# Performance work log

Measured on AMD Instinct MI355X. Metric: run time of the kernel, lower is better.

The kernel has to match this reference:

```python
import jax, jax.numpy as jnp
import numpy as np

BN_EPS = 1e-5
DIST_MIN = 1e-10


def _three_nn(p1t, p2t):
    # p1t: [B,N,3], p2t: [B,S,3] -> squared dists/idx of 3 nearest, [B,N,3]
    d2 = (jnp.sum(p1t * p1t, -1, keepdims=True)
          - 2.0 * jnp.einsum('bnc,bsc->bns', p1t, p2t)
          + jnp.sum(p2t * p2t, -1)[:, None, :])  # [B,N,S]
    neg, idx = jax.lax.top_k(-d2, 3)
    return -neg, idx


def _gather_knn(f2t, idx):
    # f2t: [B,S,D], idx: [B,N,3] -> [B,N,3,D]
    return jax.vmap(lambda f, i: f[i])(f2t, idx)


def _conv_bn_relu(x, W, b, g, beta):
    # x: [B,C,N]; 1x1 conv == channel GEMM, then train-mode BN, then ReLU
    y = jnp.einsum('oc,bcn->bon', W, x) + b[None, :, None]
    mean = jnp.mean(y, axis=(0, 2), keepdims=True)
    var = jnp.mean((y - mean) ** 2, axis=(0, 2), keepdims=True)
    yn = (y - mean) * jax.lax.rsqrt(var + BN_EPS)
    return jax.nn.relu(yn * g[None, :, None] + beta[None, :, None])


def setup_inputs() -> dict:
    key = jax.random.key(0)
    ks = jax.random.split(key, 10)
    B, N, S, D1, D2 = 4, 8192, 2048, 128, 256
    C_in, C_mid, C_out = D1 + D2, 256, 256
    inp = {
        'pos1': jax.random.normal(ks[0], (B, 3, N), jnp.float32),
        'pos2': jax.random.normal(ks[1], (B, 3, S), jnp.float32),
        'feature1': jax.random.normal(ks[2], (B, D1, N), jnp.float32),
        'feature2': jax.random.normal(ks[3], (B, D2, S), jnp.float32),
        'W1': jax.random.normal(ks[4], (C_mid, C_in), jnp.float32) / np.sqrt(C_in),
        'b1': jnp.zeros((C_mid,), jnp.float32),
        'g1': jnp.ones((C_mid,), jnp.float32),
        'beta1': jnp.zeros((C_mid,), jnp.float32),
        'W2': jax.random.normal(ks[5], (C_out, C_mid), jnp.float32) / np.sqrt(C_mid),
        'b2': jnp.zeros((C_out,), jnp.float32),
        'g2': jnp.ones((C_out,), jnp.float32),
        'beta2': jnp.zeros((C_out,), jnp.float32),
    }
    return inp


def reference(pos1, pos2, feature1, feature2, W1, b1, g1, beta1, W2, b2, g2, beta2):
    B = pos1.shape[0]
    p1t = jnp.transpose(pos1, (0, 2, 1))  # [B,N,3]
    p2t = jnp.transpose(pos2, (0, 2, 1))  # [B,S,3]
    dists, idx = _three_nn(p1t, p2t)      # [B,N,3]
    dists = jnp.maximum(dists, DIST_MIN)
    w = 1.0 / dists
    w = w / jnp.sum(w, -1, keepdims=True)  # [B,N,3]
    f2t = jnp.transpose(feature2, (0, 2, 1))  # [B,S,D2]
    gathered = _gather_knn(f2t, idx)           # [B,N,3,D2]
    interp = jnp.sum(gathered * w[..., None], axis=2)  # [B,N,D2]
    interp = jnp.transpose(interp, (0, 2, 1))          # [B,D2,N]
    feat = jnp.concatenate([interp, feature1], axis=1)  # [B,D2+D1,N]
    feat = _conv_bn_relu(feat, W1, b1, g1, beta1)
    feat = _conv_bn_relu(feat, W2, b2, g2, beta2)
    return feat
```

## Files before the change

kernel.cpp:

```cpp
#include <hip/hip_runtime.h>
#include <hip/hip_bf16.h>

constexpr int B = 4, N = 8192, S = 2048;

typedef __attribute__((ext_vector_type(8))) short short8;
typedef __attribute__((ext_vector_type(4))) float v4f;

__device__ inline float u2f(ushort u) {
    union { ushort u; __hip_bfloat16 h; } c; c.u = u; return __bfloat162float(c.h);
}
__device__ inline ushort f2u(float f) {
    union { ushort u; __hip_bfloat16 h; } c; c.h = __float2bfloat16(f); return c.u;
}
__device__ inline void async_lds16(const void* g, void* l) {
    __builtin_amdgcn_global_load_lds(
        (const __attribute__((address_space(1))) unsigned*)g,
        (__attribute__((address_space(3))) unsigned*)l, 16, 0, 0);
}
__device__ inline short8 ld8(const ushort* p) { return *(const short8*)p; }

__global__ __launch_bounds__(256) void prep_kernel(
    const float* __restrict__ W1, const float* __restrict__ W2,
    __hip_bfloat16* __restrict__ W1r, __hip_bfloat16* __restrict__ W2r,
    float* __restrict__ zero_region)
{
    int i = blockIdx.x * 256 + threadIdx.x;
    if (i < 12288) {
        int kk = i >> 10, q = (i >> 8) & 3, o = i & 255;
        const float* src = W1 + o * 384 + kk * 32 + q * 8;
        float4 a = *(const float4*)src, b = *(const float4*)(src + 4);
        union { short8 s; ushort u[8]; } pk;
        pk.u[0] = f2u(a.x); pk.u[1] = f2u(a.y); pk.u[2] = f2u(a.z); pk.u[3] = f2u(a.w);
        pk.u[4] = f2u(b.x); pk.u[5] = f2u(b.y); pk.u[6] = f2u(b.z); pk.u[7] = f2u(b.w);
        *(short8*)((ushort*)W1r + i * 8) = pk.s;
    } else if (i < 20480) {
        int u = i - 12288;
        int kk = u >> 10, q = (u >> 8) & 3, o = u & 255;
        const float* src = W2 + o * 256 + kk * 32 + q * 8;
        float4 a = *(const float4*)src, b = *(const float4*)(src + 4);
        union { short8 s; ushort u[8]; } pk;
        pk.u[0] = f2u(a.x); pk.u[1] = f2u(a.y); pk.u[2] = f2u(a.z); pk.u[3] = f2u(a.w);
        pk.u[4] = f2u(b.x); pk.u[5] = f2u(b.y); pk.u[6] = f2u(b.z); pk.u[7] = f2u(b.w);
        *(short8*)((ushort*)W2r + u * 8) = pk.s;
    } else if (i < 21504) {
        zero_region[i - 20480] = 0.f;
    }
}

__global__ __launch_bounds__(256) void knn_kernel(
    const float* __restrict__ pos1, const float* __restrict__ pos2,
    float* __restrict__ wgt, int* __restrict__ idxb)
{
    __shared__ float4 p2s[S];
    const int b = blockIdx.y;
    for (int s = threadIdx.x; s < S; s += 256) {
        float x = pos2[(b * 3 + 0) * S + s];
        float y = pos2[(b * 3 + 1) * S + s];
        float z = pos2[(b * 3 + 2) * S + s];
        p2s[s] = make_float4(x, y, z, x * x + y * y + z * z);
    }
    __syncthreads();

    const int qi = blockIdx.x * 16 + (threadIdx.x >> 4);
    const int lp = threadIdx.x & 15;
    const float x1 = pos1[(b * 3 + 0) * N + qi];
    const float y1 = pos1[(b * 3 + 1) * N + qi];
    const float z1 = pos1[(b * 3 + 2) * N + qi];
    const float t1 = x1 * x1 + y1 * y1 + z1 * z1;

    float d0 = 3.4e38f, d1 = 3.4e38f, d2 = 3.4e38f;
    int i0 = 0x7fffffff, i1 = 0x7fffffff, i2 = 0x7fffffff;

    for (int tt = 0; tt < S / 16; ++tt) {
        int s = 16 * tt + lp;
        float4 p = p2s[s];
        float dot = x1 * p.x + y1 * p.y + z1 * p.z;
        float dd = (t1 - 2.0f * dot) + p.w;
        bool c0 = dd < d0, c1 = dd < d1, c2 = dd < d2;
        d2 = c1 ? d1 : (c2 ? dd : d2);
        i2 = c1 ? i1 : (c2 ? s : i2);
        d1 = c0 ? d0 : (c1 ? dd : d1);
        i1 = c0 ? i0 : (c1 ? s : i1);
        d0 = c0 ? dd : d0;
        i0 = c0 ? s : i0;
    }

    #pragma unroll
    for (int m = 1; m <= 8; m <<= 1) {
        float c0 = __shfl_xor(d0, m), c1 = __shfl_xor(d1, m), c2 = __shfl_xor(d2, m);
        int   j0 = __shfl_xor(i0, m), j1 = __shfl_xor(i1, m), j2 = __shfl_xor(i2, m);
        float cd[3] = {c0, c1, c2};
        int   cj[3] = {j0, j1, j2};
        #pragma unroll
        for (int k = 0; k < 3; ++k) {
            float d = cd[k]; int id = cj[k];
            bool l0 = (d < d0) || (d == d0 && id < i0);
            bool l1 = (d < d1) || (d == d1 && id < i1);
            bool l2 = (d < d2) || (d == d2 && id < i2);
            if (l0)      { d2 = d1; i2 = i1; d1 = d0; i1 = i0; d0 = d; i0 = id; }
            else if (l1) { d2 = d1; i2 = i1; d1 = d; i1 = id; }
            else if (l2) { d2 = d; i2 = id; }
        }
    }

    if (lp == 0) {
        float w0 = 1.f / fmaxf(d0, 1e-10f);
        float w1 = 1.f / fmaxf(d1, 1e-10f);
        float w2 = 1.f / fmaxf(d2, 1e-10f);
        float inv = 1.f / (w0 + w1 + w2);
        i0 = ((unsigned)i0 < S) ? i0 : 0;
        i1 = ((unsigned)i1 < S) ? i1 : 0;
        i2 = ((unsigned)i2 < S) ? i2 : 0;
        int base = (b * N + qi) * 3;
        wgt[base + 0] = w0 * inv; wgt[base + 1] = w1 * inv; wgt[base + 2] = w2 * inv;
        idxb[base + 0] = i0; idxb[base + 1] = i1; idxb[base + 2] = i2;
    }
}

__global__ __launch_bounds__(256) void transpose_k(
    const float* __restrict__ in, __hip_bfloat16* __restrict__ out,
    int L, int C)
{
    __shared__ ushort tl[64][66];
    const int b = blockIdx.z;
    const int l0 = blockIdx.x * 64, c0 = blockIdx.y * 64;
    const int t = threadIdx.x;
    const float* ip = in + (size_t)b * C * L;
    const int lr = t & 63, cb = t >> 6;
    #pragma unroll
    for (int i = 0; i < 16; ++i) {
        int c = cb + 4 * i;
        tl[lr][c] = f2u(ip[(size_t)(c0 + c) * L + l0 + lr]);
    }
    __syncthreads();
    ushort* op = (ushort*)out + (size_t)b * L * C;
    const int cp = t & 31, lrow = t >> 5;
    #pragma unroll
    for (int i = 0; i < 8; ++i) {
        int l = lrow + 8 * i;
        ushort2 v;
        v.x = tl[l][2 * cp];
        v.y = tl[l][2 * cp + 1];
        *(ushort2*)(op + (size_t)(l0 + l) * C + c0 + 2 * cp) = v;
    }
}

__global__ __launch_bounds__(256) void gemm1_kernel(
    const __hip_bfloat16* __restrict__ Wr, const float* __restrict__ bias,
    const __hip_bfloat16* __restrict__ f2T, const __hip_bfloat16* __restrict__ f1T,
    const int* __restrict__ idxb, const float* __restrict__ wgt,
    __hip_bfloat16* __restrict__ y, float* __restrict__ sums)
{
    __shared__ __align__(16) ushort Xs[64 * 384];
    __shared__ __align__(16) ushort Wbuf[2 * 8192];
    const int t = threadIdx.x;
    const int b = blockIdx.y;
    const int n0 = blockIdx.x * 64;
    const int w = t >> 6, lane = t & 63;
    const int q = lane >> 4, r = lane & 15, r7 = r & 7;

    {
        const char* g0 = (const char*)Wr;
        #pragma unroll
        for (int jj = 0; jj < 4; ++jj)
            async_lds16(g0 + jj * 4096 + t * 16,
                        (char*)Wbuf + jj * 4096 + w * 1024);
    }

    {
        const int lp = t & 31, ro = t >> 5;
        #pragma unroll
        for (int it = 0; it < 8; ++it) {
            int rr = ro + 8 * it;
            int base = (b * N + n0 + rr) * 3;
            int s0 = idxb[base], s1 = idxb[base + 1], s2 = idxb[base + 2];
            s0 = ((unsigned)s0 < S) ? s0 : 0;
            s1 = ((unsigned)s1 < S) ? s1 : 0;
            s2 = ((unsigned)s2 < S) ? s2 : 0;
            float w0 = wgt[base], w1 = wgt[base + 1], w2 = wgt[base + 2];
            union { short8 s; ushort u[8]; } a, c, d, o;
            a.s = ld8((const ushort*)f2T + ((size_t)b * S + s0) * 256 + 8 * lp);
            c.s = ld8((const ushort*)f2T + ((size_t)b * S + s1) * 256 + 8 * lp);
            d.s = ld8((const ushort*)f2T + ((size_t)b * S + s2) * 256 + 8 * lp);
            #pragma unroll
            for (int j = 0; j < 8; ++j)
                o.u[j] = f2u(w0 * u2f(a.u[j]) + w1 * u2f(c.u[j]) + w2 * u2f(d.u[j]));
            *(short8*)(Xs + rr * 384 + ((lp ^ ro) * 8)) = o.s;
        }
    }
    {
        const int lp = t & 15, ro = t >> 4;
        #pragma unroll
        for (int it = 0; it < 4; ++it) {
            int rr = ro + 16 * it;
            short8 v = ld8((const ushort*)f1T + ((size_t)b * N + n0 + rr) * 128 + 8 * lp);
            int c = 32 + lp;
            *(short8*)(Xs + rr * 384 + ((c ^ (rr & 7)) * 8)) = v;
        }
    }
    __syncthreads();

    v4f acc[4][4];
    #pragma unroll
    for (int mt = 0; mt < 4; ++mt)
        #pragma unroll
        for (int nf = 0; nf < 4; ++nf) acc[mt][nf] = (v4f){0.f, 0.f, 0.f, 0.f};

    for (int kk = 0; kk < 12; ++kk) {
        if (kk < 11) {
            const char* g = (const char*)Wr + (kk + 1) * 16384;
            char* l = (char*)Wbuf + ((kk + 1) & 1) * 16384;
            #pragma unroll
            for (int jj = 0; jj < 4; ++jj)
                async_lds16(g + jj * 4096 + t * 16, l + jj * 4096 + w * 1024);
        }
        const ushort* Wb = Wbuf + (kk & 1) * 8192;
        short8 af[4], bf[4];
        #pragma unroll
        for (int mt = 0; mt < 4; ++mt)
            af[mt] = ld8(Wb + q * 2048 + (w * 64 + mt * 16 + r) * 8);
        #pragma unroll
        for (int nf = 0; nf < 4; ++nf)
            bf[nf] = ld8(Xs + (nf * 16 + r) * 384 + (((kk * 4 + q) ^ r7) * 8));
        #pragma unroll
        for (int mt = 0; mt < 4; ++mt)
            #pragma unroll
            for (int nf = 0; nf < 4; ++nf)
                acc[mt][nf] = __builtin_amdgcn_mfma_f32_16x16x32_bf16(
                    af[mt], bf[nf], acc[mt][nf], 0, 0, 0);
        __syncthreads();
    }

    float* statS = (float*)Xs;
    float* statQ = statS + 256;
    #pragma unroll
    for (int mt = 0; mt < 4; ++mt) {
        int ob = w * 64 + mt * 16 + q * 4;
        float4 bi = *(const float4*)(bias + ob);
        float sj0 = 0, sj1 = 0, sj2 = 0, sj3 = 0;
        float qj0 = 0, qj1 = 0, qj2 = 0, qj3 = 0;
        #pragma unroll
        for (int nf = 0; nf < 4; ++nf) {
            int n = n0 + nf * 16 + r;
            float v0 = acc[mt][nf][0] + bi.x, v1 = acc[mt][nf][1] + bi.y;
            float v2 = acc[mt][nf][2] + bi.z, v3 = acc[mt][nf][3] + bi.w;
            ushort4 pk; pk.x = f2u(v0); pk.y = f2u(v1); pk.z = f2u(v2); pk.w = f2u(v3);
            *(ushort4*)((ushort*)y + ((size_t)b * N + n) * 256 + ob) = pk;
            sj0 += v0; sj1 += v1; sj2 += v2; sj3 += v3;
            qj0 += v0 * v0; qj1 += v1 * v1; qj2 += v2 * v2; qj3 += v3 * v3;
        }
        #pragma unroll
        for (int m = 1; m <= 8; m <<= 1) {
            sj0 += __shfl_xor(sj0, m); sj1 += __shfl_xor(sj1, m);
            sj2 += __shfl_xor(sj2, m); sj3 += __shfl_xor(sj3, m);
            qj0 += __shfl_xor(qj0, m); qj1 += __shfl_xor(qj1, m);
            qj2 += __shfl_xor(qj2, m); qj3 += __shfl_xor(qj3, m);
        }
        if (r == 0) {
            statS[ob + 0] = sj0; statS[ob + 1] = sj1;
            statS[ob + 2] = sj2; statS[ob + 3] = sj3;
            statQ[ob + 0] = qj0; statQ[ob + 1] = qj1;
            statQ[ob + 2] = qj2; statQ[ob + 3] = qj3;
        }
    }
    __syncthreads();
    atomicAdd(&sums[t], statS[t]);
    atomicAdd(&sums[256 + t], statQ[t]);
}

__global__ __launch_bounds__(256) void gemm2_kernel(
    const __hip_bfloat16* __restrict__ Wr, const float* __restrict__ bias,
    const float* __restrict__ sums1, const float* __restrict__ g1,
    const float* __restrict__ be1,
    __hip_bfloat16* __restrict__ y, float* __restrict__ sums)
{
    __shared__ __align__(16) ushort Xs[64 * 256];
    __shared__ __align__(16) ushort Wbuf[2 * 8192];
    __shared__ float ssA[256], ssB[256];
    const int t = threadIdx.x;
    const int b = blockIdx.y;
    const int n0 = blockIdx.x * 64;
    const int w = t >> 6, lane = t & 63;
    const int q = lane >> 4, r = lane & 15, r7 = r & 7;

    {
        const char* g0 = (const char*)Wr;
        #pragma unroll
        for (int jj = 0; jj < 4; ++jj)
            async_lds16(g0 + jj * 4096 + t * 16,
                        (char*)Wbuf + jj * 4096 + w * 1024);
    }

    {
        float sv = sums1[t], qv = sums1[256 + t];
        float mean = sv * (1.f / 32768.f);
        float var = qv * (1.f / 32768.f) - mean * mean;
        float rstd = rsqrtf(var + 1e-5f);
        float sc = g1[t] * rstd;
        ssA[t] = sc;
        ssB[t] = be1[t] - mean * sc;
    }
    __syncthreads();

    {
        const int lp = t & 31, ro = t >> 5;
        #pragma unroll
        for (int it = 0; it < 8; ++it) {
            int rr = ro + 8 * it;
            union { short8 s; ushort u[8]; } v, o;
            v.s = ld8((const ushort*)y + ((size_t)b * N + n0 + rr) * 256 + 8 * lp);
            #pragma unroll
            for (int j = 0; j < 8; ++j)
                o.u[j] = f2u(fmaxf(u2f(v.u[j]) * ssA[8 * lp + j] + ssB[8 * lp + j], 0.f));
            *(short8*)(Xs + rr * 256 + ((lp ^ ro) * 8)) = o.s;
        }
    }
    __syncthreads();

    v4f acc[4][4];
    #pragma unroll
    for (int mt = 0; mt < 4; ++mt)
        #pragma unroll
        for (int nf = 0; nf < 4; ++nf) acc[mt][nf] = (v4f){0.f, 0.f, 0.f, 0.f};

    for (int kk = 0; kk < 8; ++kk) {
        if (kk < 7) {
            const char* g = (const char*)Wr + (kk + 1) * 16384;
            char* l = (char*)Wbuf + ((kk + 1) & 1) * 16384;
            #pragma unroll
            for (int jj = 0; jj < 4; ++jj)
                async_lds16(g + jj * 4096 + t * 16, l + jj * 4096 + w * 1024);
        }
        const ushort* Wb = Wbuf + (kk & 1) * 8192;
        short8 af[4], bf[4];
        #pragma unroll
        for (int mt = 0; mt < 4; ++mt)
            af[mt] = ld8(Wb + q * 2048 + (w * 64 + mt * 16 + r) * 8);
        #pragma unroll
        for (int nf = 0; nf < 4; ++nf)
            bf[nf] = ld8(Xs + (nf * 16 + r) * 256 + (((kk * 4 + q) ^ r7) * 8));
        #pragma unroll
        for (int mt = 0; mt < 4; ++mt)
            #pragma unroll
            for (int nf = 0; nf < 4; ++nf)
                acc[mt][nf] = __builtin_amdgcn_mfma_f32_16x16x32_bf16(
                    af[mt], bf[nf], acc[mt][nf], 0, 0, 0);
        __syncthreads();
    }

    float* statS = (float*)Xs;
    float* statQ = statS + 256;
    #pragma unroll
    for (int mt = 0; mt < 4; ++mt) {
        int ob = w * 64 + mt * 16 + q * 4;
        float4 bi = *(const float4*)(bias + ob);
        float sj0 = 0, sj1 = 0, sj2 = 0, sj3 = 0;
        float qj0 = 0, qj1 = 0, qj2 = 0, qj3 = 0;
        #pragma unroll
        for (int nf = 0; nf < 4; ++nf) {
            int n = n0 + nf * 16 + r;
            float v0 = acc[mt][nf][0] + bi.x, v1 = acc[mt][nf][1] + bi.y;
            float v2 = acc[mt][nf][2] + bi.z, v3 = acc[mt][nf][3] + bi.w;
            ushort4 pk; pk.x = f2u(v0); pk.y = f2u(v1); pk.z = f2u(v2); pk.w = f2u(v3);
            *(ushort4*)((ushort*)y + ((size_t)b * N + n) * 256 + ob) = pk;
            sj0 += v0; sj1 += v1; sj2 += v2; sj3 += v3;
            qj0 += v0 * v0; qj1 += v1 * v1; qj2 += v2 * v2; qj3 += v3 * v3;
        }
        #pragma unroll
        for (int m = 1; m <= 8; m <<= 1) {
            sj0 += __shfl_xor(sj0, m); sj1 += __shfl_xor(sj1, m);
            sj2 += __shfl_xor(sj2, m); sj3 += __shfl_xor(sj3, m);
            qj0 += __shfl_xor(qj0, m); qj1 += __shfl_xor(qj1, m);
            qj2 += __shfl_xor(qj2, m); qj3 += __shfl_xor(qj3, m);
        }
        if (r == 0) {
            statS[ob + 0] = sj0; statS[ob + 1] = sj1;
            statS[ob + 2] = sj2; statS[ob + 3] = sj3;
            statQ[ob + 0] = qj0; statQ[ob + 1] = qj1;
            statQ[ob + 2] = qj2; statQ[ob + 3] = qj3;
        }
    }
    __syncthreads();
    atomicAdd(&sums[t], statS[t]);
    atomicAdd(&sums[256 + t], statQ[t]);
}

__global__ __launch_bounds__(256) void final_kernel(
    const __hip_bfloat16* __restrict__ Y, const float* __restrict__ sums2,
    const float* __restrict__ g2, const float* __restrict__ be2,
    float* __restrict__ out)
{
    __shared__ float tl[64][65];
    __shared__ float ssA[64], ssB[64];
    const int t = threadIdx.x;
    const int b = blockIdx.z;
    const int n0 = blockIdx.x * 64, c0 = blockIdx.y * 64;

    if (t < 64) {
        int c = c0 + t;
        float sv = sums2[c], qv = sums2[256 + c];
        float mean = sv * (1.f / 32768.f);
        float var = qv * (1.f / 32768.f) - mean * mean;
        float rstd = rsqrtf(var + 1e-5f);
        float sc = g2[c] * rstd;
        ssA[t] = sc;
        ssB[t] = be2[c] - mean * sc;
    }
    __syncthreads();

    const int nl = t >> 3, cho = 8 * (t & 7);
    #pragma unroll
    for (int it = 0; it < 2; ++it) {
        int n = nl + 32 * it;
        union { short8 s; ushort u[8]; } v;
        v.s = ld8((const ushort*)Y + ((size_t)b * N + n0 + n) * 256 + c0 + cho);
        #pragma unroll
        for (int j = 0; j < 8; ++j)
            tl[n][cho + j] = fmaxf(u2f(v.u[j]) * ssA[cho + j] + ssB[cho + j], 0.f);
    }
    __syncthreads();

    const int cl = t >> 4, n4 = (t & 15) * 4;
    #pragma unroll
    for (int it = 0; it < 4; ++it) {
        int c = cl + 16 * it;
        float4 v;
        v.x = tl[n4 + 0][c]; v.y = tl[n4 + 1][c];
        v.z = tl[n4 + 2][c]; v.w = tl[n4 + 3][c];
        *(float4*)(out + ((size_t)b * 256 + c0 + c) * N + n0 + n4) = v;
    }
}

extern "C" void kernel_launch(void* const* d_in, const int* in_sizes, int n_in,
                              void* d_out, int out_size, void* d_ws, size_t ws_size,
                              hipStream_t stream)
{
    (void)in_sizes; (void)n_in; (void)out_size;
    if (ws_size < (30u << 20)) return;

    const float* pos1 = (const float*)d_in[0];
    const float* pos2 = (const float*)d_in[1];
    const float* f1   = (const float*)d_in[2];
    const float* f2   = (const float*)d_in[3];
    const float* W1   = (const float*)d_in[4];
    const float* b1   = (const float*)d_in[5];
    const float* g1   = (const float*)d_in[6];
    const float* be1  = (const float*)d_in[7];
    const float* W2   = (const float*)d_in[8];
    const float* b2   = (const float*)d_in[9];
    const float* g2   = (const float*)d_in[10];
    const float* be2  = (const float*)d_in[11];

    char* ws = (char*)d_ws;
    int*   idxb  = (int*)(ws + 0);
    float* wgt   = (float*)(ws + 393216);
    float* sums1 = (float*)(ws + 786432);
    float* sums2 = sums1 + 512;
    __hip_bfloat16* W1r = (__hip_bfloat16*)(ws + 819200);
    __hip_bfloat16* W2r = (__hip_bfloat16*)(ws + 1015808);
    __hip_bfloat16* f2T = (__hip_bfloat16*)(ws + (2u << 20));
    __hip_bfloat16* f1T = (__hip_bfloat16*)(ws + (6u << 20));
    __hip_bfloat16* y   = (__hip_bfloat16*)(ws + (14u << 20));

    prep_kernel<<<84, 256, 0, stream>>>(W1, W2, W1r, W2r, sums1);

    knn_kernel<<<dim3(N / 16, B), 256, 0, stream>>>(pos1, pos2, wgt, idxb);

    transpose_k<<<dim3(S / 64, 256 / 64, B), 256, 0, stream>>>(f2, f2T, S, 256);
    transpose_k<<<dim3(N / 64, 128 / 64, B), 256, 0, stream>>>(f1, f1T, N, 128);

    gemm1_kernel<<<dim3(N / 64, B), 256, 0, stream>>>(
        W1r, b1, f2T, f1T, idxb, wgt, y, sums1);
    gemm2_kernel<<<dim3(N / 64, B), 256, 0, stream>>>(
        W2r, b2, sums1, g1, be1, y, sums2);
    final_kernel<<<dim3(N / 64, 256 / 64, B), 256, 0, stream>>>(
        y, sums2, g2, be2, (float*)d_out);
}
```

Baseline: 209.7 us.

## Find three-NN threshold with branchless med3 pass, then gather indices in filtered pass

The three-nearest-neighbour search now runs in two passes. The first keeps only the three smallest distances using min and med3 instructions, with no index tracking, and reduces them across the 16 lanes to get a global third-smallest threshold. The second pass recomputes the distances and runs the indexed insertion only for candidates at or below that threshold, which should be rare and cheap. This doubles the distance computation and shared-memory reads, in exchange for a shorter dependency chain per element in each loop. Distances also now use FMAs, which can change rounding slightly.

```diff
diff --git a/kernel.cpp b/kernel.cpp
--- a/kernel.cpp
+++ b/kernel.cpp
@@ -18,6 +18,11 @@
         (__attribute__((address_space(3))) unsigned*)l, 16, 0, 0);
 }
 __device__ inline short8 ld8(const ushort* p) { return *(const short8*)p; }
+
+__device__ inline float dist2f(float4 p, float x1, float y1, float z1, float t1) {
+    float dot = fmaf(x1, p.x, fmaf(y1, p.y, z1 * p.z));
+    return fmaf(-2.f, dot, t1) + p.w;
+}
 
 __global__ __launch_bounds__(256) void prep_kernel(
     const float* __restrict__ W1, const float* __restrict__ W2,
@@ -69,44 +74,67 @@
     const float t1 = x1 * x1 + y1 * y1 + z1 * z1;
 
     float d0 = 3.4e38f, d1 = 3.4e38f, d2 = 3.4e38f;
+    #pragma unroll 4
+    for (int tt = 0; tt < S / 16; ++tt) {
+        float dd = dist2f(p2s[16 * tt + lp], x1, y1, z1, t1);
+        float a1 = __builtin_amdgcn_fmed3f(dd, d0, d1);
+        float a2 = __builtin_amdgcn_fmed3f(dd, d1, d2);
+        d0 = fminf(d0, dd);
+        d1 = a1; d2 = a2;
+    }
+    #pragma unroll
+    for (int m = 1; m <= 8; m <<= 1) {
+        float e0 = __shfl_xor(d0, m), e1 = __shfl_xor(d1, m), e2 = __shfl_xor(d2, m);
+        float es[3] = {e0, e1, e2};
+        #pragma unroll
+        for (int k = 0; k < 3; ++k) {
+            float e = es[k];
+            float a1 = __builtin_amdgcn_fmed3f(e, d0, d1);
+            float a2 = __builtin_amdgcn_fmed3f(e, d1, d2);
+            d0 = fminf(d0, e);
+            d1 = a1; d2 = a2;
+        }
+    }
+    const float d2g = d2;
+
+    float f0 = 3.4e38f, f1 = 3.4e38f, f2 = 3.4e38f;
     int i0 = 0x7fffffff, i1 = 0x7fffffff, i2 = 0x7fffffff;
-
     for (int tt = 0; tt < S / 16; ++tt) {
         int s = 16 * tt + lp;
-        float4 p = p2s[s];
-        float dot = x1 * p.x + y1 * p.y + z1 * p.z;
-        float dd = (t1 - 2.0f * dot) + p.w;
-        bool c0 = dd < d0, c1 = dd < d1, c2 = dd < d2;
-        d2 = c1 ? d1 : (c2 ? dd : d2);
-        i2 = c1 ? i1 : (c2 ? s : i2);
-        d1 = c0 ? d0 : (c1 ? dd : d1);
-        i1 = c0 ? i0 : (c1 ? s : i1);
-        d0 = c0 ? dd : d0;
-        i0 = c0 ? s : i0;
+        float dd = dist2f(p2s[s], x1, y1, z1, t1);
+        if (dd <= d2g) {
+            bool c0 = dd < f0, c1 = dd < f1, c2 = dd < f2;
+            f2 = c1 ? f1 : (c2 ? dd : f2);
+            i2 = c1 ? i1 : (c2 ? s : i2);
+            f1 = c0 ? f0 : (c1 ? dd : f1);
+            i1 = c0 ? i0 : (c1 ? s : i1);
+            f0 = c0 ? dd : f0;
+            i0 = c0 ? s : i0;
+        }
     }
 
     #pragma unroll
     for (int m = 1; m <= 8; m <<= 1) {
-        float c0 = __shfl_xor(d0, m), c1 = __shfl_xor(d1, m), c2 = __shfl_xor(d2, m);
+        float c0 = __shfl_xor(f0, m), c1 = __shfl_xor(f1, m), c2 = __shfl_xor(f2, m);
         int   j0 = __shfl_xor(i0, m), j1 = __shfl_xor(i1, m), j2 = __shfl_xor(i2, m);
         float cd[3] = {c0, c1, c2};
         int   cj[3] = {j0, j1, j2};
         #pragma unroll
         for (int k = 0; k < 3; ++k) {
             float d = cd[k]; int id = cj[k];
-            bool l0 = (d < d0) || (d == d0 && id < i0);
-            bool l1 = (d < d1) || (d == d1 && id < i1);
-            bool l2 = (d < d2) || (d == d2 && id < i2);
-            if (l0)      { d2 = d1; i2 = i1; d1 = d0; i1 = i0; d0 = d; i0 = id; }
-            else if (l1) { d2 = d1; i2 = i1; d1 = d; i1 = id; }
-            else if (l2) { d2 = d; i2 = id; }
+            bool l0 = (d < f0) || (d == f0 && id < i0);
+            bool l1 = (d < f1) || (d == f1 && id < i1);
+            bool l2 = (d < f2) || (d == f2 && id < i2);
+            if (l0)      { f2 = f1; i2 = i1; f1 = f0; i1 = i0; f0 = d; i0 = id; }
+            else if (l1) { f2 = f1; i2 = i1; f1 = d; i1 = id; }
+            else if (l2) { f2 = d; i2 = id; }
         }
     }
 
     if (lp == 0) {
-        float w0 = 1.f / fmaxf(d0, 1e-10f);
-        float w1 = 1.f / fmaxf(d1, 1e-10f);
-        float w2 = 1.f / fmaxf(d2, 1e-10f);
+        float w0 = 1.f / fmaxf(f0, 1e-10f);
+        float w1 = 1.f / fmaxf(f1, 1e-10f);
+        float w2 = 1.f / fmaxf(f2, 1e-10f);
         float inv = 1.f / (w0 + w1 + w2);
         i0 = ((unsigned)i0 < S) ? i0 : 0;
         i1 = ((unsigned)i1 < S) ? i1 : 0;
```

Measured after the change: 213.4 us. No clear change (+1.8%).

## Restructure KNN: one query per lane, waves split candidates, med3 top-3 insert

Applied to the files above, without the earlier changes.

The KNN kernel now assigns one query point per lane and splits the 2048 candidates across the four waves (512 each). Candidates are read straight from global memory with wave-uniform addresses, which become scalar/broadcast loads, so the LDS staging of pos2 goes away. The top-3 update uses fmed3/fmin instead of chained selects, and the per-wave partial lists are merged through a small LDS buffer instead of a 16-lane shuffle reduction. Distances are computed as direct differences rather than the expanded norm form, which may change tie and rounding behaviour slightly compared with the reference. The grid shrinks by a factor of four.

```diff
diff --git a/kernel.cpp b/kernel.cpp
--- a/kernel.cpp
+++ b/kernel.cpp
@@ -51,69 +51,71 @@
     const float* __restrict__ pos1, const float* __restrict__ pos2,
     float* __restrict__ wgt, int* __restrict__ idxb)
 {
-    __shared__ float4 p2s[S];
+    __shared__ float dLs[4][64][3];
+    __shared__ int   iLs[4][64][3];
     const int b = blockIdx.y;
-    for (int s = threadIdx.x; s < S; s += 256) {
-        float x = pos2[(b * 3 + 0) * S + s];
-        float y = pos2[(b * 3 + 1) * S + s];
-        float z = pos2[(b * 3 + 2) * S + s];
-        p2s[s] = make_float4(x, y, z, x * x + y * y + z * z);
-    }
-    __syncthreads();
-
-    const int qi = blockIdx.x * 16 + (threadIdx.x >> 4);
-    const int lp = threadIdx.x & 15;
+    const int t = threadIdx.x;
+    const int lane = t & 63;
+    const int w = __builtin_amdgcn_readfirstlane(t >> 6);
+    const int qi = blockIdx.x * 64 + lane;
+
     const float x1 = pos1[(b * 3 + 0) * N + qi];
     const float y1 = pos1[(b * 3 + 1) * N + qi];
     const float z1 = pos1[(b * 3 + 2) * N + qi];
-    const float t1 = x1 * x1 + y1 * y1 + z1 * z1;
+
+    const float* __restrict__ px = pos2 + (b * 3 + 0) * S + w * 512;
+    const float* __restrict__ py = pos2 + (b * 3 + 1) * S + w * 512;
+    const float* __restrict__ pz = pos2 + (b * 3 + 2) * S + w * 512;
 
     float d0 = 3.4e38f, d1 = 3.4e38f, d2 = 3.4e38f;
     int i0 = 0x7fffffff, i1 = 0x7fffffff, i2 = 0x7fffffff;
 
-    for (int tt = 0; tt < S / 16; ++tt) {
-        int s = 16 * tt + lp;
-        float4 p = p2s[s];
-        float dot = x1 * p.x + y1 * p.y + z1 * p.z;
-        float dd = (t1 - 2.0f * dot) + p.w;
+    #pragma unroll 8
+    for (int i = 0; i < 512; ++i) {
+        float qx = px[i], qy = py[i], qz = pz[i];
+        float dx = x1 - qx, dy = y1 - qy, dz = z1 - qz;
+        float dd = fmaf(dx, dx, fmaf(dy, dy, dz * dz));
+        int s = w * 512 + i;
         bool c0 = dd < d0, c1 = dd < d1, c2 = dd < d2;
-        d2 = c1 ? d1 : (c2 ? dd : d2);
         i2 = c1 ? i1 : (c2 ? s : i2);
-        d1 = c0 ? d0 : (c1 ? dd : d1);
         i1 = c0 ? i0 : (c1 ? s : i1);
-        d0 = c0 ? dd : d0;
         i0 = c0 ? s : i0;
-    }
-
-    #pragma unroll
-    for (int m = 1; m <= 8; m <<= 1) {
-        float c0 = __shfl_xor(d0, m), c1 = __shfl_xor(d1, m), c2 = __shfl_xor(d2, m);
-        int   j0 = __shfl_xor(i0, m), j1 = __shfl_xor(i1, m), j2 = __shfl_xor(i2, m);
-        float cd[3] = {c0, c1, c2};
-        int   cj[3] = {j0, j1, j2};
-        #pragma unroll
-        for (int k = 0; k < 3; ++k) {
-            float d = cd[k]; int id = cj[k];
-            bool l0 = (d < d0) || (d == d0 && id < i0);
-            bool l1 = (d < d1) || (d == d1 && id < i1);
-            bool l2 = (d < d2) || (d == d2 && id < i2);
-            if (l0)      { d2 = d1; i2 = i1; d1 = d0; i1 = i0; d0 = d; i0 = id; }
-            else if (l1) { d2 = d1; i2 = i1; d1 = d; i1 = id; }
-            else if (l2) { d2 = d; i2 = id; }
-        }
-    }
-
-    if (lp == 0) {
-        float w0 = 1.f / fmaxf(d0, 1e-10f);
-        float w1 = 1.f / fmaxf(d1, 1e-10f);
-        float w2 = 1.f / fmaxf(d2, 1e-10f);
+        float nd1 = __builtin_amdgcn_fmed3f(dd, d0, d1);
+        float nd2 = __builtin_amdgcn_fmed3f(dd, d1, d2);
+        d0 = fminf(d0, dd);
+        d1 = nd1; d2 = nd2;
+    }
+
+    dLs[w][lane][0] = d0; dLs[w][lane][1] = d1; dLs[w][lane][2] = d2;
+    iLs[w][lane][0] = i0; iLs[w][lane][1] = i1; iLs[w][lane][2] = i2;
+    __syncthreads();
+
+    if (t < 64) {
+        float f0 = dLs[0][t][0], f1 = dLs[0][t][1], f2 = dLs[0][t][2];
+        int   j0 = iLs[0][t][0], j1 = iLs[0][t][1], j2 = iLs[0][t][2];
+        #pragma unroll
+        for (int c = 1; c < 4; ++c) {
+            #pragma unroll
+            for (int k = 0; k < 3; ++k) {
+                float d = dLs[c][t][k]; int id = iLs[c][t][k];
+                bool l0 = (d < f0) || (d == f0 && id < j0);
+                bool l1 = (d < f1) || (d == f1 && id < j1);
+                bool l2 = (d < f2) || (d == f2 && id < j2);
+                if (l0)      { f2 = f1; j2 = j1; f1 = f0; j1 = j0; f0 = d; j0 = id; }
+                else if (l1) { f2 = f1; j2 = j1; f1 = d; j1 = id; }
+                else if (l2) { f2 = d; j2 = id; }
+            }
+        }
+        float w0 = 1.f / fmaxf(f0, 1e-10f);
+        float w1 = 1.f / fmaxf(f1, 1e-10f);
+        float w2 = 1.f / fmaxf(f2, 1e-10f);
         float inv = 1.f / (w0 + w1 + w2);
-        i0 = ((unsigned)i0 < S) ? i0 : 0;
-        i1 = ((unsigned)i1 < S) ? i1 : 0;
-        i2 = ((unsigned)i2 < S) ? i2 : 0;
-        int base = (b * N + qi) * 3;
+        j0 = ((unsigned)j0 < S) ? j0 : 0;
+        j1 = ((unsigned)j1 < S) ? j1 : 0;
+        j2 = ((unsigned)j2 < S) ? j2 : 0;
+        int base = (b * N + blockIdx.x * 64 + t) * 3;
         wgt[base + 0] = w0 * inv; wgt[base + 1] = w1 * inv; wgt[base + 2] = w2 * inv;
-        idxb[base + 0] = i0; idxb[base + 1] = i1; idxb[base + 2] = i2;
+        idxb[base + 0] = j0; idxb[base + 1] = j1; idxb[base + 2] = j2;
     }
 }
 
@@ -464,7 +466,7 @@
 
     prep_kernel<<<84, 256, 0, stream>>>(W1, W2, W1r, W2r, sums1);
 
-    knn_kernel<<<dim3(N / 16, B), 256, 0, stream>>>(pos1, pos2, wgt, idxb);
+    knn_kernel<<<dim3(N / 64, B), 256, 0, stream>>>(pos1, pos2, wgt, idxb);
 
     transpose_k<<<dim3(S / 64, 256 / 64, B), 256, 0, stream>>>(f2, f2T, S, 256);
     transpose_k<<<dim3(N / 64, 128 / 64, B), 256, 0, stream>>>(f1, f1T, N, 128);
```

Result: no change. 210.2 us (+0.2%).
